# Kernel optimization log

Hardware: AMD Instinct MI355X
Metric: run time of the kernel (lower is better)

## Reference

```python
import jax, jax.numpy as jnp
import numpy as np

HD = 256          # hidden_dim[0]
KF = 2            # k factor
KD = HD * KF      # 512, bilinear feature dim
L = 2000          # hard-coded sequence length
B = 4
NEG = np.float32(np.finfo(np.float32).min)  # finite min, NOT -inf (matches torch code)
EPS = 1e-5


def _fc(x, V, g, b):
    # weight_norm(Linear, dim=None): W = g * V / ||V||_F, then ReLU
    W = (g / jnp.linalg.norm(V)) * V  # [KD, HD]
    return jax.nn.relu(jnp.einsum('blh,kh->blk', x, W) + b)


def setup_inputs() -> dict:
    key = jax.random.key(0)
    ks = jax.random.split(key, 12)
    X = jax.random.normal(ks[0], (B, L, HD), dtype=jnp.float32)
    Y = jax.random.normal(ks[1], (B, L, HD), dtype=jnp.float32)
    mask1 = jax.random.bernoulli(ks[2], 0.8, (B, L)).astype(jnp.float32)
    mask2 = jax.random.bernoulli(ks[3], 0.8, (B, L)).astype(jnp.float32)
    # Q_net / K_net params (single weight-normed linear each)
    Qv = jax.random.normal(ks[4], (KD, HD), dtype=jnp.float32) * 0.05
    Qg = jnp.asarray(1.0, dtype=jnp.float32)
    Qb = jax.random.normal(ks[5], (KD,), dtype=jnp.float32) * 0.05
    Kv = jax.random.normal(ks[6], (KD, HD), dtype=jnp.float32) * 0.05
    Kg = jnp.asarray(1.0, dtype=jnp.float32)
    Kb = jax.random.normal(ks[7], (KD,), dtype=jnp.float32) * 0.05
    h_mat = jax.random.normal(ks[8], (KD,), dtype=jnp.float32)   # (1,1,KD) squeezed
    h_bias = jax.random.normal(ks[9], (), dtype=jnp.float32)     # (1,1,1) squeezed
    gamma = jnp.ones((KD,), dtype=jnp.float32)                   # BatchNorm1d affine
    beta = jnp.zeros((KD,), dtype=jnp.float32)
    return {"X": X, "Y": Y, "mask1": mask1, "mask2": mask2,
            "Qv": Qv, "Qg": Qg, "Qb": Qb, "Kv": Kv, "Kg": Kg, "Kb": Kb,
            "h_mat": h_mat, "h_bias": h_bias, "gamma": gamma, "beta": beta}


def _masked_softmax(A, m_row):
    # m_row: [B,1,L], broadcasts over axis 1; softmax over dim 1 as in torch
    logits = jnp.where(m_row > 0, A, NEG)
    att = jax.nn.softmax(logits, axis=1)
    return m_row * att


def reference(X, Y, mask1, mask2, Qv, Qg, Qb, Kv, Kg, Kb, h_mat, h_bias, gamma, beta):
    A1_X = _fc(X, Qv, Qg, Qb)  # [B,L,KD]
    A1_Y = _fc(Y, Kv, Kg, Kb)
    A2_Y = _fc(Y, Qv, Qg, Qb)
    A2_X = _fc(X, Kv, Kg, Kb)
    # bilinear co-attention maps [B,L,L]
    A1 = jnp.einsum('bvk,bqk->bvq', A1_X * h_mat, A1_Y) + h_bias
    A2 = jnp.einsum('bqk,bvk->bqv', A2_Y * h_mat, A2_X) + h_bias
    m1r = mask1[:, None, :]  # mask1_attend[b,v,q] = mask1[b,q]
    m2r = mask2[:, None, :]
    alpha = _masked_softmax(A1, m2r)
    logits_X = jnp.einsum('bvq,bqk->bvk', alpha, A1_Y) * mask1[:, :, None]
    beta_att = _masked_softmax(A2, m1r)
    logits_Y = jnp.einsum('bqv,bvk->bqk', beta_att, A2_X) * mask2[:, :, None]
    # AvgPool2d((2000,1)) == mean over sequence dim
    pooled = logits_X.mean(axis=1) + logits_Y.mean(axis=1)  # [B,KD]
    # BatchNorm1d training-mode forward (biased batch stats)
    mu = pooled.mean(axis=0)
    var = pooled.var(axis=0)
    return gamma * (pooled - mu) * jax.lax.rsqrt(var + EPS) + beta
```

## Files before the change

### kernel.cpp

```cpp
#include <hip/hip_runtime.h>

#define NB 4
#define LSEQ 2000
#define HD 256
#define KD 512
#define LPAD 2048
#define SMALL_N 18562

using short8 = __attribute__((ext_vector_type(8))) short;
using f32x4  = __attribute__((ext_vector_type(4))) float;
typedef unsigned short u16;

__device__ __forceinline__ float b2f(u16 u) { return __uint_as_float(((unsigned)u) << 16); }
__device__ __forceinline__ u16 f2b(float f) {
    unsigned u = __float_as_uint(f);
    u += 0x7FFFu + ((u >> 16) & 1u);
    return (u16)(u >> 16);
}
__device__ __forceinline__ bool detect32(const void* gamma) {
    return ((const float*)gamma)[0] == 1.0f;
}
__device__ __forceinline__ void gl_lds16(const u16* g, short* l) {
    __builtin_amdgcn_global_load_lds(
        (const __attribute__((address_space(1))) unsigned int*)g,
        (__attribute__((address_space(3))) unsigned int*)l, 16, 0, 0);
}

__global__ void convert_kernel(const void* X, const void* Y, const void* Qv, const void* Kv,
                               const void* m1, const void* m2, const void* Qb, const void* Kb,
                               const void* hm, const void* Qg, const void* Kg,
                               const void* gamma, const void* beta,
                               u16* __restrict__ Xb, u16* __restrict__ Yb,
                               u16* __restrict__ Qvb, u16* __restrict__ Kvb,
                               float* __restrict__ smallf, float* __restrict__ ssq)
{
    const bool is32 = detect32(gamma);
    const int seg = blockIdx.y;
    if (seg < 4) {
        const void* src = seg == 0 ? X : seg == 1 ? Y : seg == 2 ? Qv : Kv;
        u16* dst = seg == 0 ? Xb : seg == 1 ? Yb : seg == 2 ? Qvb : Kvb;
        const int n = (seg < 2) ? NB * LSEQ * HD : KD * HD;
        const int i0 = (blockIdx.x * 256 + threadIdx.x) * 8;
        if (i0 >= n) return;
        uint4 pack;
        u16* v = (u16*)&pack;
        if (is32) {
            float4 fa = ((const float4*)src)[(i0 >> 2)];
            float4 fb = ((const float4*)src)[(i0 >> 2) + 1];
            v[0] = f2b(fa.x); v[1] = f2b(fa.y); v[2] = f2b(fa.z); v[3] = f2b(fa.w);
            v[4] = f2b(fb.x); v[5] = f2b(fb.y); v[6] = f2b(fb.z); v[7] = f2b(fb.w);
        } else {
            pack = ((const uint4*)src)[i0 >> 3];
        }
        ((uint4*)dst)[i0 >> 3] = pack;
        if (seg >= 2) {
            float s = 0.f;
            #pragma unroll
            for (int j = 0; j < 8; ++j) { float f = b2f(v[j]); s = fmaf(f, f, s); }
            #pragma unroll
            for (int off = 32; off > 0; off >>= 1) s += __shfl_xor(s, off);
            if ((threadIdx.x & 63) == 0) atomicAdd(&ssq[seg - 2], s);
        }
    } else {
        const int i0 = (blockIdx.x * 256 + threadIdx.x) * 4;
        for (int i = i0; i < i0 + 4; ++i) {
            if (i >= SMALL_N) break;
            const void* src; int off;
            if      (i <  8000) { src = m1;    off = i; }
            else if (i < 16000) { src = m2;    off = i - 8000; }
            else if (i < 16512) { src = Qb;    off = i - 16000; }
            else if (i < 17024) { src = Kb;    off = i - 16512; }
            else if (i < 17536) { src = hm;    off = i - 17024; }
            else if (i < 18048) { src = gamma; off = i - 17536; }
            else if (i < 18560) { src = beta;  off = i - 18048; }
            else if (i == 18560) {
                float f = ((const float*)Qg)[0];
                smallf[i] = (f == 1.0f) ? 1.0f : b2f(((const u16*)Qg)[0]);
                continue;
            } else {
                float f = ((const float*)Kg)[0];
                smallf[i] = (f == 1.0f) ? 1.0f : b2f(((const u16*)Kg)[0]);
                continue;
            }
            smallf[i] = is32 ? ((const float*)src)[off] : b2f(((const u16*)src)[off]);
        }
    }
}

__global__ __launch_bounds__(512, 2)
void fc_kernel(const u16* __restrict__ X, const u16* __restrict__ Y,
               const u16* __restrict__ Qv, const u16* __restrict__ Kv,
               const float* __restrict__ Qbf, const float* __restrict__ Kbf,
               const float* __restrict__ hf, const float* __restrict__ gv,
               const float* __restrict__ ssq, u16* __restrict__ fcout)
{
    const int mt = blockIdx.x, nt = blockIdx.y, t = blockIdx.z;
    const int b = t >> 2, which = t & 3;
    const u16* In = ((which == 0) | (which == 3)) ? (X + (size_t)b * LSEQ * HD)
                                                  : (Y + (size_t)b * LSEQ * HD);
    const bool isQ = (which == 0) | (which == 2);
    const u16* W      = isQ ? Qv : Kv;
    const float* bias = isQ ? Qbf : Kbf;
    const int j0 = isQ ? 0 : 1;
    const float s = gv[j0] / sqrtf(ssq[j0]);
    u16* out = fcout + (size_t)t * LSEQ * KD;

    __shared__ __align__(16) short AL[4][256 * 32];
    __shared__ __align__(16) short BL[4][256 * 32];

    const int tid = threadIdx.x;
    const int lane = tid & 63, wave = tid >> 6;
    const int wm = wave >> 2, wn = wave & 3;
    const int quad = lane >> 4, l15 = lane & 15;
    const int r0 = mt * 256, n0 = nt * 256;

    const int srow = tid >> 2;
    const int kslot = (tid & 3) ^ ((tid >> 3) & 3);
    int grA0 = min(r0 + srow, LSEQ - 1), grA1 = min(r0 + 128 + srow, LSEQ - 1);
    const u16* pAa = In + (size_t)grA0 * HD + kslot * 8;
    const u16* pAb = In + (size_t)grA1 * HD + kslot * 8;
    const u16* pBa = W + (size_t)(n0 + srow) * HD + kslot * 8;
    const u16* pBb = W + (size_t)(n0 + 128 + srow) * HD + kslot * 8;
    const int ldst = tid * 8;
    const int swz = (quad ^ ((l15 >> 1) & 3)) * 8;

    #define STAGE_A(h) { short* d_ = &AL[(h) & 3][ldst];               \
                         gl_lds16(pAa + (h) * 32, d_);                 \
                         gl_lds16(pAb + (h) * 32, d_ + 4096); }
    #define STAGE_B(h) { short* d_ = &BL[(h) & 3][ldst];               \
                         gl_lds16(pBa + (h) * 32, d_);                 \
                         gl_lds16(pBb + (h) * 32, d_ + 4096); }

    STAGE_A(0); STAGE_B(0); STAGE_A(1); STAGE_B(1); STAGE_A(2); STAGE_B(2);
    asm volatile("s_waitcnt vmcnt(4)" ::: "memory");
    __builtin_amdgcn_s_barrier();
    __builtin_amdgcn_sched_barrier(0);

    f32x4 acc[8][4] = {};
    short8 bf[4];

    #pragma unroll
    for (int kt = 0; kt < 4; ++kt) {
        #pragma unroll
        for (int p = 0; p < 4; ++p) {
            const int j = 2 * kt + (p >> 1);
            const short* Ab = AL[j & 3];
            const short* Bb = BL[j & 3];
            short8 af[4];
            #pragma unroll
            for (int mi = 0; mi < 4; ++mi) {
                int lr = wm * 128 + (p & 1) * 64 + mi * 16 + l15;
                af[mi] = *(const short8*)&Ab[lr * 32 + swz];
            }
            if ((p & 1) == 0) {
                #pragma unroll
                for (int ni = 0; ni < 4; ++ni) {
                    int lc = wn * 64 + ni * 16 + l15;
                    bf[ni] = *(const short8*)&Bb[lc * 32 + swz];
                }
            }
            if (p == 0)      { if (2 * kt + 3 <= 7) STAGE_A(2 * kt + 3); }
            else if (p == 1) { if (2 * kt + 3 <= 7) STAGE_B(2 * kt + 3); }
            else if (p == 2) { if (2 * kt + 4 <= 7) STAGE_A(2 * kt + 4); }
            else {
                if (2 * kt + 4 <= 7) STAGE_B(2 * kt + 4);
                if (kt < 2)       asm volatile("s_waitcnt vmcnt(4)" ::: "memory");
                else if (kt == 2) asm volatile("s_waitcnt vmcnt(0)" ::: "memory");
            }
            asm volatile("" ::: "memory");
            __builtin_amdgcn_s_barrier();
            __builtin_amdgcn_sched_barrier(0);
            __builtin_amdgcn_s_setprio(1);
            #pragma unroll
            for (int mi = 0; mi < 4; ++mi)
                #pragma unroll
                for (int ni = 0; ni < 4; ++ni)
                    acc[(p & 1) * 4 + mi][ni] =
                        __builtin_amdgcn_mfma_f32_16x16x32_bf16(af[mi], bf[ni],
                                                                acc[(p & 1) * 4 + mi][ni], 0, 0, 0);
            __builtin_amdgcn_s_setprio(0);
            asm volatile("" ::: "memory");
            __builtin_amdgcn_s_barrier();
            __builtin_amdgcn_sched_barrier(0);
        }
    }

    #pragma unroll
    for (int ni = 0; ni < 4; ++ni) {
        int n = n0 + wn * 64 + ni * 16 + l15;
        float bv = bias[n];
        float hv = isQ ? hf[n] : 1.0f;
        #pragma unroll
        for (int aq = 0; aq < 8; ++aq) {
            int mb = r0 + wm * 128 + (aq >> 2) * 64 + (aq & 3) * 16 + quad * 4;
            #pragma unroll
            for (int r = 0; r < 4; ++r) {
                int m = mb + r;
                if (m < LSEQ) {
                    float v = fmaf(s, acc[aq][ni][r], bv);
                    v = v > 0.f ? v : 0.f;
                    out[(size_t)m * KD + n] = f2b(v * hv);
                }
            }
        }
    }
    #undef STAGE_A
    #undef STAGE_B
}

__global__ __launch_bounds__(512, 2)
void colsm_kernel(const u16* __restrict__ fc, const float* __restrict__ m1f,
                  const float* __restrict__ m2f,
                  float* __restrict__ part_d, float* __restrict__ part_n)
{
    const int lin = blockIdx.x;
    const int half = lin >> 8, idx = lin & 255;
    const int xcd = idx & 7, slot = idx >> 3;
    const int z  = 4 * half + (xcd >> 1);
    const int vs = 4 * (xcd & 1) + (slot & 3);
    const int qt = slot >> 2;
    const int a = z >> 2, b = z & 3;
    const u16* R  = fc + (size_t)(b * 4 + (a == 0 ? 1 : 3)) * LSEQ * KD;
    const u16* Sm = fc + (size_t)(b * 4 + (a == 0 ? 0 : 2)) * LSEQ * KD;
    const float* wmask = (a == 0 ? m1f : m2f) + (size_t)b * LSEQ;

    __shared__ __align__(16) short AL[4][256 * 32];
    __shared__ __align__(16) short BL[4][256 * 32];

    const int tid = threadIdx.x;
    const int lane = tid & 63, wave = tid >> 6;
    const int wm = wave >> 2, wn = wave & 3;
    const int quad = lane >> 4, l15 = lane & 15;
    const int r0 = qt * 256, c0 = vs * 256;

    const int srow = tid >> 2;
    const int kslot = (tid & 3) ^ ((tid >> 3) & 3);
    int grA0 = min(r0 + srow, LSEQ - 1), grA1 = min(r0 + 128 + srow, LSEQ - 1);
    int gcB0 = min(c0 + srow, LSEQ - 1), gcB1 = min(c0 + 128 + srow, LSEQ - 1);
    const u16* pRa = R  + (size_t)grA0 * KD + kslot * 8;
    const u16* pRb = R  + (size_t)grA1 * KD + kslot * 8;
    const u16* pSa = Sm + (size_t)gcB0 * KD + kslot * 8;
    const u16* pSb = Sm + (size_t)gcB1 * KD + kslot * 8;
    const int ldst = tid * 8;
    const int swz = (quad ^ ((l15 >> 1) & 3)) * 8;

    #define STAGE_A(h) { short* d_ = &AL[(h) & 3][ldst];               \
                         gl_lds16(pRa + (h) * 32, d_);                 \
                         gl_lds16(pRb + (h) * 32, d_ + 4096); }
    #define STAGE_B(h) { short* d_ = &BL[(h) & 3][ldst];               \
                         gl_lds16(pSa + (h) * 32, d_);                 \
                         gl_lds16(pSb + (h) * 32, d_ + 4096); }

    STAGE_A(0); STAGE_B(0); STAGE_A(1); STAGE_B(1); STAGE_A(2); STAGE_B(2);
    asm volatile("s_waitcnt vmcnt(4)" ::: "memory");
    __builtin_amdgcn_s_barrier();
    __builtin_amdgcn_sched_barrier(0);

    f32x4 acc[8][4] = {};
    short8 bf[4];

    #pragma unroll 2
    for (int t = 0; t < 8; ++t) {
        #pragma unroll
        for (int p = 0; p < 4; ++p) {
            const int j = 2 * t + (p >> 1);
            const short* Ab = AL[j & 3];
            const short* Bb = BL[j & 3];
            short8 af[4];
            #pragma unroll
            for (int mi = 0; mi < 4; ++mi) {
                int lr = wm * 128 + (p & 1) * 64 + mi * 16 + l15;
                af[mi] = *(const short8*)&Ab[lr * 32 + swz];
            }
            if ((p & 1) == 0) {
                #pragma unroll
                for (int ni = 0; ni < 4; ++ni) {
                    int lc = wn * 64 + ni * 16 + l15;
                    bf[ni] = *(const short8*)&Bb[lc * 32 + swz];
                }
            }
            if (p == 0)      { if (2 * t + 3 <= 15) STAGE_A(2 * t + 3); }
            else if (p == 1) { if (2 * t + 3 <= 15) STAGE_B(2 * t + 3); }
            else if (p == 2) { if (2 * t + 4 <= 15) STAGE_A(2 * t + 4); }
            else {
                if (2 * t + 4 <= 15) STAGE_B(2 * t + 4);
                if (t < 6)       asm volatile("s_waitcnt vmcnt(4)" ::: "memory");
                else if (t == 6) asm volatile("s_waitcnt vmcnt(0)" ::: "memory");
            }
            asm volatile("" ::: "memory");
            __builtin_amdgcn_s_barrier();
            __builtin_amdgcn_sched_barrier(0);
            __builtin_amdgcn_s_setprio(1);
            #pragma unroll
            for (int mi = 0; mi < 4; ++mi)
                #pragma unroll
                for (int ni = 0; ni < 4; ++ni)
                    acc[(p & 1) * 4 + mi][ni] =
                        __builtin_amdgcn_mfma_f32_16x16x32_bf16(af[mi], bf[ni],
                                                                acc[(p & 1) * 4 + mi][ni], 0, 0, 0);
            __builtin_amdgcn_s_setprio(0);
            asm volatile("" ::: "memory");
            __builtin_amdgcn_s_barrier();
            __builtin_amdgcn_sched_barrier(0);
        }
    }

    __syncthreads();
    float* ldsD = (float*)&AL[0][0];
    float* ldsN = (float*)&AL[1][0];

    float wv[4], vv[4];
    #pragma unroll
    for (int ni = 0; ni < 4; ++ni) {
        int cg = c0 + wn * 64 + ni * 16 + l15;
        bool valid = cg < LSEQ;
        vv[ni] = valid ? 1.f : 0.f;
        wv[ni] = valid ? wmask[min(cg, LSEQ - 1)] : 0.f;
    }
    #pragma unroll
    for (int aq = 0; aq < 8; ++aq)
        #pragma unroll
        for (int r = 0; r < 4; ++r) {
            float d = 0.f, nn = 0.f;
            #pragma unroll
            for (int ni = 0; ni < 4; ++ni) {
                float e = __expf(acc[aq][ni][r]);
                d = fmaf(vv[ni], e, d);
                nn = fmaf(wv[ni], e, nn);
            }
            #pragma unroll
            for (int off = 1; off < 16; off <<= 1) {
                d += __shfl_xor(d, off);
                nn += __shfl_xor(nn, off);
            }
            if (l15 == 0) {
                int row = wm * 128 + (aq >> 2) * 64 + (aq & 3) * 16 + quad * 4 + r;
                ldsD[row * 4 + wn] = d;
                ldsN[row * 4 + wn] = nn;
            }
        }
    __syncthreads();
    if (tid < 256) {
        int q = r0 + tid;
        if (q < LSEQ) {
            size_t p = ((size_t)(z * 8 + vs)) * LPAD + q;
            part_d[p] = ldsD[tid * 4 + 0] + ldsD[tid * 4 + 1] + ldsD[tid * 4 + 2] + ldsD[tid * 4 + 3];
            part_n[p] = ldsN[tid * 4 + 0] + ldsN[tid * 4 + 1] + ldsN[tid * 4 + 2] + ldsN[tid * 4 + 3];
        }
    }
    #undef STAGE_A
    #undef STAGE_B
}

__global__ void pooled_kernel(const u16* __restrict__ fc,
                              const float* __restrict__ part_d, const float* __restrict__ part_n,
                              const float* __restrict__ m1f, const float* __restrict__ m2f,
                              float* __restrict__ pp)
{
    const int b = blockIdx.x, rs = blockIdx.y;
    const int tid = threadIdx.x;
    const int rbeg = rs * 50;
    __shared__ float c1s[50], c2s[50];
    if (tid < 50) {
        int r = rbeg + tid;
        float d = 0.f, n = 0.f;
        #pragma unroll
        for (int vs = 0; vs < 8; ++vs) {
            size_t p = ((size_t)(b * 8 + vs)) * LPAD + r;
            d += part_d[p]; n += part_n[p];
        }
        c1s[tid] = m2f[b * LSEQ + r] * n / d;
    } else if (tid >= 64 && tid < 114) {
        int i = tid - 64, r = rbeg + i;
        float d = 0.f, n = 0.f;
        #pragma unroll
        for (int vs = 0; vs < 8; ++vs) {
            size_t p = ((size_t)((4 + b) * 8 + vs)) * LPAD + r;
            d += part_d[p]; n += part_n[p];
        }
        c2s[i] = m1f[b * LSEQ + r] * n / d;
    }
    __syncthreads();
    const int k = tid;
    const u16* YK = fc + (size_t)(b * 4 + 1) * LSEQ * KD;
    const u16* XK = fc + (size_t)(b * 4 + 3) * LSEQ * KD;
    float s = 0.f;
    for (int i = 0; i < 50; ++i) {
        int r = rbeg + i;
        s = fmaf(c1s[i], b2f(YK[(size_t)r * KD + k]), s);
        s = fmaf(c2s[i], b2f(XK[(size_t)r * KD + k]), s);
    }
    pp[((size_t)b * 40 + rs) * KD + k] = s;
}

__global__ void ln_kernel(const float* __restrict__ pp, const float* __restrict__ gammaf,
                          const float* __restrict__ betaf, const void* __restrict__ gamma_orig,
                          void* __restrict__ out)
{
    int k = blockIdx.x * 256 + threadIdx.x;
    float p[NB];
    #pragma unroll
    for (int b = 0; b < NB; ++b) {
        float s = 0.f;
        for (int rs = 0; rs < 40; ++rs) s += pp[((size_t)b * 40 + rs) * KD + k];
        p[b] = s * (1.0f / LSEQ);
    }
    float mu = 0.25f * (p[0] + p[1] + p[2] + p[3]);
    float var = 0.f;
    #pragma unroll
    for (int b = 0; b < NB; ++b) { float d = p[b] - mu; var = fmaf(d, d, var); }
    var *= 0.25f;
    float inv = rsqrtf(var + 1e-5f);
    float g = gammaf[k], be = betaf[k];
    const bool is32 = detect32(gamma_orig);
    #pragma unroll
    for (int b = 0; b < NB; ++b) {
        float v = fmaf(g * (p[b] - mu), inv, be);
        if (is32) ((float*)out)[b * KD + k] = v;
        else      ((u16*)out)[b * KD + k] = f2b(v);
    }
}

extern "C" void kernel_launch(void* const* d_in, const int* in_sizes, int n_in,
                              void* d_out, int out_size, void* d_ws, size_t ws_size,
                              hipStream_t stream)
{
    const void* X  = d_in[0];
    const void* Y  = d_in[1];
    const void* m1 = d_in[2];
    const void* m2 = d_in[3];
    const void* Qv = d_in[4];
    const void* Qg = d_in[5];
    const void* Qb = d_in[6];
    const void* Kv = d_in[7];
    const void* Kg = d_in[8];
    const void* Kb = d_in[9];
    const void* h  = d_in[10];
    const void* gamma = d_in[12];
    const void* beta  = d_in[13];

    char* ws = (char*)d_ws;
    size_t off = 0;
    u16* Xb  = (u16*)(ws + off); off += (size_t)NB * LSEQ * HD * 2;
    u16* Yb  = (u16*)(ws + off); off += (size_t)NB * LSEQ * HD * 2;
    u16* Qvb = (u16*)(ws + off); off += (size_t)KD * HD * 2;
    u16* Kvb = (u16*)(ws + off); off += (size_t)KD * HD * 2;
    float* smallf = (float*)(ws + off); off += ((size_t)(SMALL_N + 2) * 4 + 15) / 16 * 16;
    u16* fc  = (u16*)(ws + off); off += (size_t)16 * LSEQ * KD * 2;
    float* part_d = (float*)(ws + off); off += (size_t)8 * 8 * LPAD * 4;
    float* part_n = (float*)(ws + off); off += (size_t)8 * 8 * LPAD * 4;
    float* pp     = (float*)(ws + off); off += (size_t)NB * 40 * KD * 4;

    const float* m1f = smallf;
    const float* m2f = smallf + 8000;
    const float* Qbf = smallf + 16000;
    const float* Kbf = smallf + 16512;
    const float* hf  = smallf + 17024;
    const float* gmf = smallf + 17536;
    const float* bef = smallf + 18048;
    const float* gv  = smallf + 18560;
    float* ssq = smallf + SMALL_N;

    hipMemsetAsync(ssq, 0, 2 * sizeof(float), stream);
    convert_kernel<<<dim3(1000, 5), 256, 0, stream>>>(X, Y, Qv, Kv, m1, m2, Qb, Kb, h, Qg, Kg,
                                                      gamma, beta, Xb, Yb, Qvb, Kvb, smallf, ssq);
    fc_kernel     <<<dim3(8, 2, 16), 512, 0, stream>>>(Xb, Yb, Qvb, Kvb, Qbf, Kbf, hf, gv, ssq, fc);
    colsm_kernel  <<<512, 512, 0, stream>>>(fc, m1f, m2f, part_d, part_n);
    pooled_kernel <<<dim3(4, 40), 512, 0, stream>>>(fc, part_d, part_n, m1f, m2f, pp);
    ln_kernel     <<<2, 256, 0, stream>>>(pp, gmf, bef, gamma, d_out);
}
```

Measured before the change: 188.0 us.

## Replace LDS-staged pipelined GEMM in colsm kernel with direct global fragment loads

Removes the four-stage global-to-LDS pipeline with barriers from colsm_kernel and has each wave load its MFMA A/B fragments directly from global memory (relying on cache) inside a simple K loop. LDS is now used only for the small row-sum reduction, and launch bounds drop to one block per CU. This removes barrier and LDS-staging overhead, but loses data sharing between waves and explicit latency hiding, so it depends on L1/L2 absorbing the redundant fragment reads.

```diff
diff --git a/kernel.cpp b/kernel.cpp
--- a/kernel.cpp
+++ b/kernel.cpp
@@ -208,15 +208,15 @@
     #undef STAGE_B
 }
 
-__global__ __launch_bounds__(512, 2)
+__global__ __launch_bounds__(512, 1)
 void colsm_kernel(const u16* __restrict__ fc, const float* __restrict__ m1f,
                   const float* __restrict__ m2f,
                   float* __restrict__ part_d, float* __restrict__ part_n)
 {
     const int lin = blockIdx.x;
-    const int half = lin >> 8, idx = lin & 255;
+    const int half_ = lin >> 8, idx = lin & 255;
     const int xcd = idx & 7, slot = idx >> 3;
-    const int z  = 4 * half + (xcd >> 1);
+    const int z  = 4 * half_ + (xcd >> 1);
     const int vs = 4 * (xcd & 1) + (slot & 3);
     const int qt = slot >> 2;
     const int a = z >> 2, b = z & 3;
@@ -224,8 +224,8 @@
     const u16* Sm = fc + (size_t)(b * 4 + (a == 0 ? 0 : 2)) * LSEQ * KD;
     const float* wmask = (a == 0 ? m1f : m2f) + (size_t)b * LSEQ;
 
-    __shared__ __align__(16) short AL[4][256 * 32];
-    __shared__ __align__(16) short BL[4][256 * 32];
+    __shared__ float ldsD[256][4];
+    __shared__ float ldsN[256][4];
 
     const int tid = threadIdx.x;
     const int lane = tid & 63, wave = tid >> 6;
@@ -233,81 +233,46 @@
     const int quad = lane >> 4, l15 = lane & 15;
     const int r0 = qt * 256, c0 = vs * 256;
 
-    const int srow = tid >> 2;
-    const int kslot = (tid & 3) ^ ((tid >> 3) & 3);
-    int grA0 = min(r0 + srow, LSEQ - 1), grA1 = min(r0 + 128 + srow, LSEQ - 1);
-    int gcB0 = min(c0 + srow, LSEQ - 1), gcB1 = min(c0 + 128 + srow, LSEQ - 1);
-    const u16* pRa = R  + (size_t)grA0 * KD + kslot * 8;
-    const u16* pRb = R  + (size_t)grA1 * KD + kslot * 8;
-    const u16* pSa = Sm + (size_t)gcB0 * KD + kslot * 8;
-    const u16* pSb = Sm + (size_t)gcB1 * KD + kslot * 8;
-    const int ldst = tid * 8;
-    const int swz = (quad ^ ((l15 >> 1) & 3)) * 8;
-
-    #define STAGE_A(h) { short* d_ = &AL[(h) & 3][ldst];               \
-                         gl_lds16(pRa + (h) * 32, d_);                 \
-                         gl_lds16(pRb + (h) * 32, d_ + 4096); }
-    #define STAGE_B(h) { short* d_ = &BL[(h) & 3][ldst];               \
-                         gl_lds16(pSa + (h) * 32, d_);                 \
-                         gl_lds16(pSb + (h) * 32, d_ + 4096); }
-
-    STAGE_A(0); STAGE_B(0); STAGE_A(1); STAGE_B(1); STAGE_A(2); STAGE_B(2);
-    asm volatile("s_waitcnt vmcnt(4)" ::: "memory");
-    __builtin_amdgcn_s_barrier();
-    __builtin_amdgcn_sched_barrier(0);
+    const u16* ap[2][4];
+    #pragma unroll
+    for (int h = 0; h < 2; ++h)
+        #pragma unroll
+        for (int mi = 0; mi < 4; ++mi) {
+            int ar = min(r0 + wm * 128 + h * 64 + mi * 16 + l15, LSEQ - 1);
+            ap[h][mi] = R + (size_t)ar * KD + quad * 8;
+        }
+    const u16* bp[4];
+    #pragma unroll
+    for (int ni = 0; ni < 4; ++ni) {
+        int br = min(c0 + wn * 64 + ni * 16 + l15, LSEQ - 1);
+        bp[ni] = Sm + (size_t)br * KD + quad * 8;
+    }
 
     f32x4 acc[8][4] = {};
-    short8 bf[4];
 
     #pragma unroll 2
-    for (int t = 0; t < 8; ++t) {
-        #pragma unroll
-        for (int p = 0; p < 4; ++p) {
-            const int j = 2 * t + (p >> 1);
-            const short* Ab = AL[j & 3];
-            const short* Bb = BL[j & 3];
-            short8 af[4];
-            #pragma unroll
-            for (int mi = 0; mi < 4; ++mi) {
-                int lr = wm * 128 + (p & 1) * 64 + mi * 16 + l15;
-                af[mi] = *(const short8*)&Ab[lr * 32 + swz];
-            }
-            if ((p & 1) == 0) {
-                #pragma unroll
-                for (int ni = 0; ni < 4; ++ni) {
-                    int lc = wn * 64 + ni * 16 + l15;
-                    bf[ni] = *(const short8*)&Bb[lc * 32 + swz];
-                }
-            }
-            if (p == 0)      { if (2 * t + 3 <= 15) STAGE_A(2 * t + 3); }
-            else if (p == 1) { if (2 * t + 3 <= 15) STAGE_B(2 * t + 3); }
-            else if (p == 2) { if (2 * t + 4 <= 15) STAGE_A(2 * t + 4); }
-            else {
-                if (2 * t + 4 <= 15) STAGE_B(2 * t + 4);
-                if (t < 6)       asm volatile("s_waitcnt vmcnt(4)" ::: "memory");
-                else if (t == 6) asm volatile("s_waitcnt vmcnt(0)" ::: "memory");
-            }
-            asm volatile("" ::: "memory");
-            __builtin_amdgcn_s_barrier();
-            __builtin_amdgcn_sched_barrier(0);
-            __builtin_amdgcn_s_setprio(1);
-            #pragma unroll
-            for (int mi = 0; mi < 4; ++mi)
-                #pragma unroll
-                for (int ni = 0; ni < 4; ++ni)
-                    acc[(p & 1) * 4 + mi][ni] =
-                        __builtin_amdgcn_mfma_f32_16x16x32_bf16(af[mi], bf[ni],
-                                                                acc[(p & 1) * 4 + mi][ni], 0, 0, 0);
-            __builtin_amdgcn_s_setprio(0);
-            asm volatile("" ::: "memory");
-            __builtin_amdgcn_s_barrier();
-            __builtin_amdgcn_sched_barrier(0);
-        }
-    }
-
-    __syncthreads();
-    float* ldsD = (float*)&AL[0][0];
-    float* ldsN = (float*)&AL[1][0];
+    for (int f = 0; f < 16; ++f) {
+        const int ko = f * 32;
+        short8 bf[4], af0[4], af1[4];
+        #pragma unroll
+        for (int ni = 0; ni < 4; ++ni) bf[ni]  = *(const short8*)(bp[ni]    + ko);
+        #pragma unroll
+        for (int mi = 0; mi < 4; ++mi) af0[mi] = *(const short8*)(ap[0][mi] + ko);
+        #pragma unroll
+        for (int mi = 0; mi < 4; ++mi) af1[mi] = *(const short8*)(ap[1][mi] + ko);
+        #pragma unroll
+        for (int mi = 0; mi < 4; ++mi)
+            #pragma unroll
+            for (int ni = 0; ni < 4; ++ni)
+                acc[mi][ni] = __builtin_amdgcn_mfma_f32_16x16x32_bf16(af0[mi], bf[ni],
+                                                                      acc[mi][ni], 0, 0, 0);
+        #pragma unroll
+        for (int mi = 0; mi < 4; ++mi)
+            #pragma unroll
+            for (int ni = 0; ni < 4; ++ni)
+                acc[4 + mi][ni] = __builtin_amdgcn_mfma_f32_16x16x32_bf16(af1[mi], bf[ni],
+                                                                          acc[4 + mi][ni], 0, 0, 0);
+    }
 
     float wv[4], vv[4];
     #pragma unroll
@@ -335,8 +300,8 @@
             }
             if (l15 == 0) {
                 int row = wm * 128 + (aq >> 2) * 64 + (aq & 3) * 16 + quad * 4 + r;
-                ldsD[row * 4 + wn] = d;
-                ldsN[row * 4 + wn] = nn;
+                ldsD[row][wn] = d;
+                ldsN[row][wn] = nn;
             }
         }
     __syncthreads();
@@ -344,12 +309,10 @@
         int q = r0 + tid;
         if (q < LSEQ) {
             size_t p = ((size_t)(z * 8 + vs)) * LPAD + q;
-            part_d[p] = ldsD[tid * 4 + 0] + ldsD[tid * 4 + 1] + ldsD[tid * 4 + 2] + ldsD[tid * 4 + 3];
-            part_n[p] = ldsN[tid * 4 + 0] + ldsN[tid * 4 + 1] + ldsN[tid * 4 + 2] + ldsN[tid * 4 + 3];
-        }
-    }
-    #undef STAGE_A
-    #undef STAGE_B
+            part_d[p] = ldsD[tid][0] + ldsD[tid][1] + ldsD[tid][2] + ldsD[tid][3];
+            part_n[p] = ldsN[tid][0] + ldsN[tid][1] + ldsN[tid][2] + ldsN[tid][3];
+        }
+    }
 }
 
 __global__ void pooled_kernel(const u16* __restrict__ fc,
```

New measurement: 240.6 us. +28.0%, slower.
